# Performance work log

Hardware: AMD Instinct MI355X
Metric: run time of the kernel (lower is better)

The kernel has to match this reference:

```python
import jax, jax.numpy as jnp
import numpy as np

N_NODES = 50000
N_EDGES = 800000
IN_CH = 64
OUT_CH = 64
PRIOR_VAR = 1.0


def setup_inputs() -> dict:
    key = jax.random.key(0)
    ks = jax.random.split(key, 10)
    mean = jax.random.normal(ks[0], (N_NODES, IN_CH), dtype=jnp.float32)
    std = jax.random.uniform(ks[1], (N_NODES, IN_CH), dtype=jnp.float32)
    edge_index = jax.random.randint(ks[2], (2, N_EDGES), 0, N_NODES, dtype=jnp.int32)
    edge_weight = jax.random.uniform(ks[3], (N_EDGES,), dtype=jnp.float32)
    # Bayesian GCN parameters (xavier-ish mu, log_sigma init -3.0) for mean- and std-branches
    scale = float(np.sqrt(6.0 / (IN_CH + OUT_CH)))
    mu_mean = jax.random.uniform(ks[4], (IN_CH, OUT_CH), minval=-scale, maxval=scale, dtype=jnp.float32)
    log_sigma_mean = jnp.full((IN_CH, OUT_CH), -3.0, dtype=jnp.float32)
    mu_std = jax.random.uniform(ks[5], (IN_CH, OUT_CH), minval=-scale, maxval=scale, dtype=jnp.float32)
    log_sigma_std = jnp.full((IN_CH, OUT_CH), -3.0, dtype=jnp.float32)
    # reparameterization noise (drawn once so reference is deterministic)
    eps_mean = jax.random.normal(ks[6], (IN_CH, OUT_CH), dtype=jnp.float32)
    eps_std = jax.random.normal(ks[7], (IN_CH, OUT_CH), dtype=jnp.float32)
    return {
        "mean": mean, "std": std, "edge_index": edge_index, "edge_weight": edge_weight,
        "mu_mean": mu_mean, "log_sigma_mean": log_sigma_mean, "eps_mean": eps_mean,
        "mu_std": mu_std, "log_sigma_std": log_sigma_std, "eps_std": eps_std,
    }


def _gcn_propagate(x, weight, edge_index, edge_weight):
    # support = x @ W; then gather src rows, scale by edge_weight, scatter-add to dst
    support = jnp.matmul(x, weight)                      # [N, out]
    src, dst = edge_index[0], edge_index[1]
    msg = edge_weight[:, None] * support[src]            # [E, out]
    return jax.ops.segment_sum(msg, dst, num_segments=N_NODES)


def _kl(mu, log_sigma):
    pv = PRIOR_VAR
    kl = 0.5 * (jnp.exp(2.0 * log_sigma) / pv + mu ** 2 / pv
                - 2.0 * log_sigma - jnp.log(jnp.asarray(pv, mu.dtype)) - 1.0)
    return kl.sum()


def reference(mean, std, edge_index, edge_weight,
              mu_mean, log_sigma_mean, eps_mean,
              mu_std, log_sigma_std, eps_std):
    # mean branch
    w_mean = mu_mean + eps_mean * jnp.exp(log_sigma_mean)
    new_mean = _gcn_propagate(mean, w_mean, edge_index, edge_weight)
    kl_mean = _kl(mu_mean, log_sigma_mean)
    # std branch operates on variance with squared edge weights
    var = std ** 2
    w_std = mu_std + eps_std * jnp.exp(log_sigma_std)
    new_log_var = _gcn_propagate(var, w_std, edge_index, edge_weight ** 2)
    kl_std = _kl(mu_std, log_sigma_std)
    new_std = jnp.sqrt(jnp.exp(new_log_var) + 1e-6)
    total_kl = kl_mean + kl_std
    return (new_mean, new_std, total_kl)
```

## Files before the change

kernel.cpp:

```cpp
#include <hip/hip_runtime.h>

#define N_NODES 50000
#define N_EDGES 800000
#define CH 64
#define OUT_OFF_STD (N_NODES * CH)
#define OUT_OFF_KL  (2 * N_NODES * CH)
#define CAP 64
#define CAP_USE 62

#define NGRP 8
#define NPG 6250
#define EPT 4
#define FILL_BLOCKS 782
#define GEMM_BLOCKS 782
#define GATHER_BLOCKS 2048
#define GWAVES_PG 1024
#define ZERO_GRID 208

typedef __attribute__((ext_vector_type(8))) short short8;
typedef __attribute__((ext_vector_type(4))) float f32x4;

__device__ __forceinline__ int rl_i(unsigned v, int lane) {
    return __builtin_amdgcn_readlane((int)v, lane);
}
__device__ __forceinline__ unsigned f2bf(float f) {
    unsigned u = __float_as_uint(f);
    return (u + 0x7fffu + ((u >> 16) & 1u)) >> 16;
}
__device__ __forceinline__ int* cnt_ptr(uint2* bins, int node) {
    return (int*)(bins + (size_t)node * CAP + 63);
}

__global__ __launch_bounds__(256) void wkl_kernel(
    const float* __restrict__ mu_m, const float* __restrict__ ls_m,
    const float* __restrict__ eps_m,
    const float* __restrict__ mu_s, const float* __restrict__ ls_s,
    const float* __restrict__ eps_s,
    unsigned short* __restrict__ fragBm, unsigned short* __restrict__ fragBv,
    float* __restrict__ kl_out, uint2* __restrict__ bins)
{
    if (blockIdx.x != 0) {
        if (blockIdx.x < 8) return;
        const int g = blockIdx.x & (NGRP - 1);
        const int loc = ((int)(blockIdx.x >> 3) - 1) * 256 + (int)threadIdx.x;
        if (loc < NPG) *cnt_ptr(bins, g * NPG + loc) = 0;
        return;
    }
    __shared__ unsigned short Wm[CH * CH];
    __shared__ unsigned short Wv[CH * CH];
    float kl = 0.0f;
    for (int i = threadIdx.x; i < CH * CH; i += 256) {
        float mu = mu_m[i], ls = ls_m[i];
        Wm[i] = (unsigned short)f2bf(mu + eps_m[i] * expf(ls));
        kl += 0.5f * (expf(2.0f * ls) + mu * mu - 2.0f * ls - 1.0f);
        mu = mu_s[i]; ls = ls_s[i];
        Wv[i] = (unsigned short)f2bf(mu + eps_s[i] * expf(ls));
        kl += 0.5f * (expf(2.0f * ls) + mu * mu - 2.0f * ls - 1.0f);
    }
    __syncthreads();
    for (int f = threadIdx.x; f < CH * CH; f += 256) {
        int j = f & 7, l = (f >> 3) & 63, ch = f >> 9;
        int k = (ch & 1) * 32 + ((l >> 4) & 3) * 8 + j;
        int n = (ch >> 1) * 16 + (l & 15);
        fragBm[f] = Wm[k * CH + n];
        fragBv[f] = Wv[k * CH + n];
    }
    for (int off = 32; off > 0; off >>= 1)
        kl += __shfl_down(kl, off, 64);
    __shared__ float red[4];
    if ((threadIdx.x & 63) == 0) red[threadIdx.x >> 6] = kl;
    __syncthreads();
    if (threadIdx.x == 0)
        kl_out[0] = red[0] + red[1] + red[2] + red[3];
}

__global__ __launch_bounds__(256) void gemfill_kernel(
    const float* __restrict__ mean, const float* __restrict__ stdv,
    const unsigned short* __restrict__ fragBm,
    const unsigned short* __restrict__ fragBv,
    const int* __restrict__ ei, const float* __restrict__ ew,
    uint2* __restrict__ bins, unsigned* __restrict__ sup)
{
    const int tid = threadIdx.x;

    if (blockIdx.x < FILL_BLOCKS) {
        const int base = (int)blockIdx.x * (256 * EPT) + tid * EPT;

        int d[EPT], s[EPT]; float w[EPT];
        if (base + EPT <= N_EDGES) {
            int4 dv = *(const int4*)(ei + N_EDGES + base);
            d[0] = dv.x; d[1] = dv.y; d[2] = dv.z; d[3] = dv.w;
            int4 sv = *(const int4*)(ei + base);
            s[0] = sv.x; s[1] = sv.y; s[2] = sv.z; s[3] = sv.w;
            float4 wv = *(const float4*)(ew + base);
            w[0] = wv.x; w[1] = wv.y; w[2] = wv.z; w[3] = wv.w;
        } else {
#pragma unroll
            for (int t = 0; t < EPT; ++t) {
                bool v = (base + t) < N_EDGES;
                d[t] = v ? ei[N_EDGES + base + t] : -1;
                s[t] = v ? ei[base + t] : 0;
                w[t] = v ? ew[base + t] : 0.0f;
            }
        }

        int slot[EPT];
#pragma unroll
        for (int t = 0; t < EPT; ++t) {
            bool act = (unsigned)d[t] < (unsigned)N_NODES;
            slot[t] = act ? atomicAdd(cnt_ptr(bins, d[t]), 1) : CAP;
        }
#pragma unroll
        for (int t = 0; t < EPT; ++t) {
            if (slot[t] < CAP_USE)
                bins[(size_t)d[t] * CAP + slot[t]] =
                    make_uint2((unsigned)s[t], __float_as_uint(w[t]));
        }
        return;
    }

    const int lane = tid & 63, wave = tid >> 6;
    const int row0 = (blockIdx.x - FILL_BLOCKS) * 64 + wave * 16;
    if (row0 >= N_NODES) return;

    const int m = lane & 15;
    const int q = (lane >> 4) & 3;
    const float* mrow = mean + (size_t)(row0 + m) * CH + q * 8;
    const float* srow = stdv + (size_t)(row0 + m) * CH + q * 8;

    short8 aM[2], aV[2];
#pragma unroll
    for (int h = 0; h < 2; ++h) {
        float4 x0 = *(const float4*)(mrow + h * 32);
        float4 x1 = *(const float4*)(mrow + h * 32 + 4);
        float4 s0 = *(const float4*)(srow + h * 32);
        float4 s1 = *(const float4*)(srow + h * 32 + 4);
        aM[h][0] = (short)f2bf(x0.x); aM[h][1] = (short)f2bf(x0.y);
        aM[h][2] = (short)f2bf(x0.z); aM[h][3] = (short)f2bf(x0.w);
        aM[h][4] = (short)f2bf(x1.x); aM[h][5] = (short)f2bf(x1.y);
        aM[h][6] = (short)f2bf(x1.z); aM[h][7] = (short)f2bf(x1.w);
        aV[h][0] = (short)f2bf(s0.x * s0.x); aV[h][1] = (short)f2bf(s0.y * s0.y);
        aV[h][2] = (short)f2bf(s0.z * s0.z); aV[h][3] = (short)f2bf(s0.w * s0.w);
        aV[h][4] = (short)f2bf(s1.x * s1.x); aV[h][5] = (short)f2bf(s1.y * s1.y);
        aV[h][6] = (short)f2bf(s1.z * s1.z); aV[h][7] = (short)f2bf(s1.w * s1.w);
    }

    f32x4 accM[4], accV[4];
#pragma unroll
    for (int c = 0; c < 4; ++c) {
        accM[c] = (f32x4)0.0f;
        accV[c] = (f32x4)0.0f;
    }
#pragma unroll
    for (int c = 0; c < 4; ++c) {
#pragma unroll
        for (int h = 0; h < 2; ++h) {
            short8 bm = *(const short8*)(fragBm + ((c * 2 + h) * 64 + lane) * 8);
            short8 bv = *(const short8*)(fragBv + ((c * 2 + h) * 64 + lane) * 8);
            accM[c] = __builtin_amdgcn_mfma_f32_16x16x32_bf16(aM[h], bm, accM[c], 0, 0, 0);
            accV[c] = __builtin_amdgcn_mfma_f32_16x16x32_bf16(aV[h], bv, accV[c], 0, 0, 0);
        }
    }

    const int rg = lane >> 4;
#pragma unroll
    for (int c = 0; c < 4; ++c) {
#pragma unroll
        for (int r = 0; r < 4; ++r) {
            int node = row0 + rg * 4 + r;
            sup[(size_t)node * CH + c * 16 + m] =
                f2bf(accM[c][r]) | (f2bf(accV[c][r]) << 16);
        }
    }
}

__global__ __launch_bounds__(256) void gather_kernel(
    const uint2* __restrict__ bins,
    const unsigned* __restrict__ sup, float* __restrict__ out)
{
    const int g = blockIdx.x & (NGRP - 1);
    const int wid = ((int)(blockIdx.x >> 3)) * 4 + (int)(threadIdx.x >> 6);
    const int col = threadIdx.x & 63;
    const int nbase = g * NPG;

    int loc = wid;
    if (loc >= NPG) return;

    uint2 pnext = bins[(size_t)(nbase + loc) * CAP + col];

    for (; loc < NPG; loc += GWAVES_PG) {
        uint2 p = pnext;
        {
            int loc2 = loc + GWAVES_PG;
            if (loc2 < NPG)
                pnext = bins[(size_t)(nbase + loc2) * CAP + col];
        }
        int cnt = rl_i(p.x, 63);
        if (cnt > CAP_USE) cnt = CAP_USE;

        float accM = 0.0f, accV = 0.0f;
        if (cnt > 0) {
            unsigned q[24];
#pragma unroll
            for (int t = 0; t < 24; ++t) {
                int e = (t < cnt) ? t : (cnt - 1);
                q[t] = sup[(size_t)(unsigned)rl_i(p.x, e) * CH + col];
            }
#pragma unroll
            for (int t = 0; t < 24; ++t) {
                int e = (t < cnt) ? t : (cnt - 1);
                float wt = (t < cnt)
                    ? __uint_as_float((unsigned)rl_i(p.y, e)) : 0.0f;
                accM += wt * __uint_as_float(q[t] << 16);
                accV += (wt * wt) * __uint_as_float(q[t] & 0xFFFF0000u);
            }
            for (int i = 24; i < cnt; i += 8) {
                unsigned qq[8]; float ww[8];
#pragma unroll
                for (int t = 0; t < 8; ++t) {
                    int e = (i + t < cnt) ? (i + t) : (cnt - 1);
                    qq[t] = sup[(size_t)(unsigned)rl_i(p.x, e) * CH + col];
                    ww[t] = (i + t < cnt)
                        ? __uint_as_float((unsigned)rl_i(p.y, e)) : 0.0f;
                }
#pragma unroll
                for (int t = 0; t < 8; ++t) {
                    accM += ww[t] * __uint_as_float(qq[t] << 16);
                    accV += (ww[t] * ww[t]) * __uint_as_float(qq[t] & 0xFFFF0000u);
                }
            }
        }
        const int n = nbase + loc;
        __builtin_nontemporal_store(accM, &out[(size_t)n * CH + col]);
        __builtin_nontemporal_store(sqrtf(expf(accV) + 1e-6f),
                                    &out[OUT_OFF_STD + (size_t)n * CH + col]);
    }
}

extern "C" void kernel_launch(void* const* d_in, const int* in_sizes, int n_in,
                              void* d_out, int out_size, void* d_ws, size_t ws_size,
                              hipStream_t stream)
{
    const float* mean  = (const float*)d_in[0];
    const float* stdv  = (const float*)d_in[1];
    const int*   ei    = (const int*)d_in[2];
    const float* ew    = (const float*)d_in[3];
    const float* mu_m  = (const float*)d_in[4];
    const float* ls_m  = (const float*)d_in[5];
    const float* eps_m = (const float*)d_in[6];
    const float* ls_s  = (const float*)d_in[8];
    const float* mu_s  = (const float*)d_in[7];
    const float* eps_s = (const float*)d_in[9];

    float* out = (float*)d_out;
    unsigned*       sup    = (unsigned*)d_ws;
    uint2*          bins   = (uint2*)(sup + (size_t)N_NODES * CH);
    unsigned short* fragBm = (unsigned short*)(bins + (size_t)N_NODES * CAP);
    unsigned short* fragBv = fragBm + CH * CH;

    wkl_kernel<<<ZERO_GRID, 256, 0, stream>>>(
        mu_m, ls_m, eps_m, mu_s, ls_s, eps_s,
        fragBm, fragBv, out + OUT_OFF_KL, bins);
    gemfill_kernel<<<FILL_BLOCKS + GEMM_BLOCKS, 256, 0, stream>>>(
        mean, stdv, fragBm, fragBv, ei, ew, bins, sup);
    gather_kernel<<<GATHER_BLOCKS, 256, 0, stream>>>(bins, sup, out);
}
```

Measured before the change: 187.9 us.

## Partition edge binning by destination node group across fill blocks

The edge fill phase now launches 8 blocks per edge chunk. Each block handles only the edges whose destination falls in its node group of 6250 nodes, so every group of blocks touches one-eighth of the bins array. The aim is better cache locality for the atomic counters and bin writes, likely within one XCD's L2. In exchange, every edge is read 8 times, and the fill block count grows, which adds load traffic.

New measurement: 175.7 us. -6.5%, faster.

```diff
diff --git a/kernel.cpp b/kernel.cpp
--- a/kernel.cpp
+++ b/kernel.cpp
@@ -10,8 +10,9 @@
 
 #define NGRP 8
 #define NPG 6250
-#define EPT 4
-#define FILL_BLOCKS 782
+#define FILL_CHUNK 2048
+#define FILL_CHUNKS 391
+#define FILL_BLOCKS (NGRP * FILL_CHUNKS)
 #define GEMM_BLOCKS 782
 #define GATHER_BLOCKS 2048
 #define GWAVES_PG 1024
@@ -84,19 +85,28 @@
     const int tid = threadIdx.x;
 
     if (blockIdx.x < FILL_BLOCKS) {
-        const int base = (int)blockIdx.x * (256 * EPT) + tid * EPT;
-
-        int d[EPT], s[EPT]; float w[EPT];
-        if (base + EPT <= N_EDGES) {
-            int4 dv = *(const int4*)(ei + N_EDGES + base);
-            d[0] = dv.x; d[1] = dv.y; d[2] = dv.z; d[3] = dv.w;
-            int4 sv = *(const int4*)(ei + base);
-            s[0] = sv.x; s[1] = sv.y; s[2] = sv.z; s[3] = sv.w;
-            float4 wv = *(const float4*)(ew + base);
-            w[0] = wv.x; w[1] = wv.y; w[2] = wv.z; w[3] = wv.w;
+        const int g = blockIdx.x & (NGRP - 1);
+        const int chunk = blockIdx.x >> 3;
+        const int base = chunk * FILL_CHUNK + tid * 8;
+        const int lo = g * NPG;
+
+        int d[8], s[8]; float w[8];
+        if (base + 8 <= N_EDGES) {
+            int4 d0 = *(const int4*)(ei + N_EDGES + base);
+            int4 d1 = *(const int4*)(ei + N_EDGES + base + 4);
+            d[0] = d0.x; d[1] = d0.y; d[2] = d0.z; d[3] = d0.w;
+            d[4] = d1.x; d[5] = d1.y; d[6] = d1.z; d[7] = d1.w;
+            int4 s0 = *(const int4*)(ei + base);
+            int4 s1 = *(const int4*)(ei + base + 4);
+            s[0] = s0.x; s[1] = s0.y; s[2] = s0.z; s[3] = s0.w;
+            s[4] = s1.x; s[5] = s1.y; s[6] = s1.z; s[7] = s1.w;
+            float4 w0 = *(const float4*)(ew + base);
+            float4 w1 = *(const float4*)(ew + base + 4);
+            w[0] = w0.x; w[1] = w0.y; w[2] = w0.z; w[3] = w0.w;
+            w[4] = w1.x; w[5] = w1.y; w[6] = w1.z; w[7] = w1.w;
         } else {
 #pragma unroll
-            for (int t = 0; t < EPT; ++t) {
+            for (int t = 0; t < 8; ++t) {
                 bool v = (base + t) < N_EDGES;
                 d[t] = v ? ei[N_EDGES + base + t] : -1;
                 s[t] = v ? ei[base + t] : 0;
@@ -104,14 +114,14 @@
             }
         }
 
-        int slot[EPT];
-#pragma unroll
-        for (int t = 0; t < EPT; ++t) {
-            bool act = (unsigned)d[t] < (unsigned)N_NODES;
+        int slot[8];
+#pragma unroll
+        for (int t = 0; t < 8; ++t) {
+            bool act = (unsigned)(d[t] - lo) < (unsigned)NPG;
             slot[t] = act ? atomicAdd(cnt_ptr(bins, d[t]), 1) : CAP;
         }
 #pragma unroll
-        for (int t = 0; t < EPT; ++t) {
+        for (int t = 0; t < 8; ++t) {
             if (slot[t] < CAP_USE)
                 bins[(size_t)d[t] * CAP + slot[t]] =
                     make_uint2((unsigned)s[t], __float_as_uint(w[t]));
```
